# Performance work log

Hardware: AMD Instinct MI355X
Metric: run time of the kernel (lower is better)

The kernel has to match this reference:

```python
import jax, jax.numpy as jnp
import numpy as np

N_PART = 2048
N_BINS = 16
N_FREQS = 8
N_BLOCKS = 4
N_HEADS = 8
DIM = 256
HID = 512
LOWER = 0.0
UPPER = 1.0
FIXED_IDXS = np.array([0, 1])
CHANGED_IDXS = np.array([2])
N_FIXED = 2
N_CHANGED = 1
EMB_IN = 2 * N_FREQS * N_FIXED + 3   # 35
AFF_OUT = N_CHANGED * (3 * N_BINS + 1)  # 49
MIN_BIN = 1e-4
MIN_SLOPE = 1e-4


def _mlp(x, W0, b0, W1, b1, W2, b2):
    # equinox MLP: depth=2 hidden layers, relu activation, identity final
    x = jax.nn.relu(x @ W0.T + b0)
    x = jax.nn.relu(x @ W1.T + b1)
    return x @ W2.T + b2


def _attention(x, Wq, Wk, bk, Wv, Wo, bo):
    # eqx.nn.MultiheadAttention: query bias off, key bias on, value bias off, output bias on
    S, D = x.shape
    dh = D // N_HEADS
    q = (x @ Wq.T).reshape(S, N_HEADS, dh)
    k = (x @ Wk.T + bk).reshape(S, N_HEADS, dh)
    v = (x @ Wv.T).reshape(S, N_HEADS, dh)
    logits = jnp.einsum('shd,thd->hst', q, k) / float(np.sqrt(dh))
    attn = jax.nn.softmax(logits, axis=-1)
    o = jnp.einsum('hst,thd->shd', attn, v).reshape(S, D)
    return o @ Wo.T + bo


def _circular(x, lower, upper, n_freqs):
    # periodic sin/cos embedding of coordinates on [lower, upper)
    freqs = 2.0 * jnp.pi * jnp.arange(1, n_freqs + 1, dtype=x.dtype) / (upper - lower)
    ang = (x - lower)[..., None] * freqs  # (rows, n_fixed, n_freqs)
    feats = jnp.concatenate([jnp.cos(ang), jnp.sin(ang)], axis=-1)
    return feats.reshape(x.shape[0], -1)  # (rows, 2*n_freqs*n_fixed)


def _rqs_forward(x, params):
    # distrax-style rational quadratic spline, boundary_slopes='circular'
    nb = N_BINS
    uw = params[..., :nb]
    uh = params[..., nb:2 * nb]
    ud = params[..., 2 * nb:]
    ud = jnp.concatenate([ud[..., :-1], ud[..., :1]], axis=-1)  # circular: last slope = first
    total = UPPER - LOWER
    widths = jax.nn.softmax(uw, axis=-1) * (total - nb * MIN_BIN) + MIN_BIN
    heights = jax.nn.softmax(uh, axis=-1) * (total - nb * MIN_BIN) + MIN_BIN
    offset = float(np.log(np.expm1(1.0 - MIN_SLOPE)))  # softplus(0+offset)+min = 1
    slopes = jax.nn.softplus(ud + offset) + MIN_SLOPE
    zero = jnp.zeros(widths.shape[:-1] + (1,), widths.dtype)
    xpos = LOWER + jnp.concatenate([zero, jnp.cumsum(widths, -1)], -1)   # (..., nb+1)
    ypos = LOWER + jnp.concatenate([zero, jnp.cumsum(heights, -1)], -1)
    inside = (x >= LOWER) & (x <= UPPER)
    xc = jnp.clip(x, LOWER, UPPER)
    k = jnp.clip(jnp.sum(xc[..., None] >= xpos, axis=-1) - 1, 0, nb - 1)
    g = lambda a: jnp.take_along_axis(a, k[..., None], axis=-1)[..., 0]
    xk, xk1 = g(xpos[..., :-1]), g(xpos[..., 1:])
    yk, yk1 = g(ypos[..., :-1]), g(ypos[..., 1:])
    dk, dk1 = g(slopes[..., :-1]), g(slopes[..., 1:])
    w = xk1 - xk
    h = yk1 - yk
    s = h / w
    z = (xc - xk) / w
    z1 = 1.0 - z
    den = s + (dk1 + dk - 2.0 * s) * z * z1
    y = yk + h * (s * z * z + dk * z * z1) / den
    logdet = 2.0 * jnp.log(s) + jnp.log(dk1 * z * z + 2.0 * s * z * z1 + dk * z1 * z1) - 2.0 * jnp.log(den)
    y = jnp.where(inside, y, x)
    logdet = jnp.where(inside, logdet, 0.0)
    return y, logdet


def _forward(pos, scale, press, temp,
             e_w0, e_b0, e_w1, e_b1, e_w2, e_b2,
             Wq, Wk, bk, Wv, Wo, bo,
             mw0, mb0, mw1, mb1, mw2, mb2,
             a_w0, a_b0, a_w1, a_b1, a_w2, a_b2):
    fixed = pos[1:, FIXED_IDXS]      # (N-1, 2)
    changed = pos[1:, CHANGED_IDXS]  # (N-1, 1)
    feats = _circular(fixed[:, FIXED_IDXS], LOWER, UPPER, N_FREQS)  # (N-1, 32)
    rows = feats.shape[0]
    ones = jnp.ones((rows, 1), feats.dtype)
    cond = jnp.concatenate([feats, ones * scale, ones * temp, ones * press], axis=-1)  # (N-1, 35)
    h = _mlp(cond, e_w0, e_b0, e_w1, e_b1, e_w2, e_b2)  # (N-1, DIM)
    for i in range(N_BLOCKS):
        h = h + _attention(h, Wq[i], Wk[i], bk[i], Wv[i], Wo[i], bo[i])
        h = h + _mlp(h, mw0[i], mb0[i], mw1[i], mb1[i], mw2[i], mb2[i])
    params = _mlp(h, a_w0, a_b0, a_w1, a_b1, a_w2, a_b2)
    params = params.reshape(N_PART - 1, N_CHANGED, 3 * N_BINS + 1)
    y, logdet = _rqs_forward(changed, params)
    pos = pos.at[1:, CHANGED_IDXS].set(y.reshape(N_PART - 1, N_CHANGED))
    return pos, logdet.sum()


def setup_inputs():
    kit = iter(jax.random.split(jax.random.key(0), 40))
    nk = lambda: next(kit)
    def W(out_d, in_d, pre=()):
        return jax.random.normal(nk(), pre + (out_d, in_d), jnp.float32) / np.sqrt(in_d)
    def b(out_d, pre=()):
        return 0.01 * jax.random.normal(nk(), pre + (out_d,), jnp.float32)
    B = (N_BLOCKS,)
    return dict(
        pos=jax.random.uniform(nk(), (N_PART, 3), jnp.float32),
        scale=jax.random.uniform(nk(), (), jnp.float32),
        press=jax.random.uniform(nk(), (), jnp.float32),
        temp=jax.random.uniform(nk(), (), jnp.float32),
        e_w0=W(HID, EMB_IN), e_b0=b(HID),
        e_w1=W(HID, HID), e_b1=b(HID),
        e_w2=W(DIM, HID), e_b2=b(DIM),
        Wq=W(DIM, DIM, B), Wk=W(DIM, DIM, B), bk=b(DIM, B),
        Wv=W(DIM, DIM, B), Wo=W(DIM, DIM, B), bo=b(DIM, B),
        mw0=W(HID, DIM, B), mb0=b(HID, B),
        mw1=W(HID, HID, B), mb1=b(HID, B),
        mw2=W(DIM, HID, B), mb2=b(DIM, B),
        a_w0=W(HID, DIM), a_b0=b(HID),
        a_w1=W(HID, HID), a_b1=b(HID),
        a_w2=W(AFF_OUT, HID), a_b2=b(AFF_OUT),
    )


def reference(pos, scale, press, temp,
              e_w0, e_b0, e_w1, e_b1, e_w2, e_b2,
              Wq, Wk, bk, Wv, Wo, bo,
              mw0, mb0, mw1, mb1, mw2, mb2,
              a_w0, a_b0, a_w1, a_b1, a_w2, a_b2):
    return _forward(pos, scale, press, temp,
                    e_w0, e_b0, e_w1, e_b1, e_w2, e_b2,
                    Wq, Wk, bk, Wv, Wo, bo,
                    mw0, mb0, mw1, mb1, mw2, mb2,
                    a_w0, a_b0, a_w1, a_b1, a_w2, a_b2)
```

## Files before the change

### kernel.cpp

```cpp
#include <hip/hip_runtime.h>
#include <math.h>

#define S_ROWS 2047
#define DIM 256
#define HID 512
#define NHEADS 8
#define DH 32
#define NBINS 16
#define AFF_OUT 49

typedef short bf16x8 __attribute__((ext_vector_type(8)));
typedef float f32x4 __attribute__((ext_vector_type(4)));
typedef float f32x16 __attribute__((ext_vector_type(16)));
typedef unsigned short u16x8 __attribute__((ext_vector_type(8)));
typedef unsigned short u16x4 __attribute__((ext_vector_type(4)));

__device__ inline unsigned short f2b(float f) {
    unsigned int u = __float_as_uint(f);
    u += 0x7FFFu + ((u >> 16) & 1u);
    return (unsigned short)(u >> 16);
}

#define W_MAIN 3957248
#define EW0P_N 32768
#define P0 (W_MAIN / 4)
#define P1 (P0 + EW0P_N / 4)
#define P2 (P1 + 2048 * 64 / 4)
#define P3 (P2 + 1537)
__global__ __launch_bounds__(256) void setup_kernel(
    const float* __restrict__ pos, const float* __restrict__ scale,
    const float* __restrict__ press, const float* __restrict__ temp,
    const float* __restrict__ e_w0, const float* __restrict__ p0,
    const float* __restrict__ p1, const float* __restrict__ p2,
    const float* __restrict__ p3, const float* __restrict__ p4,
    const float* __restrict__ p5, const float* __restrict__ p6,
    const float* __restrict__ p7, const float* __restrict__ p8,
    const float* __restrict__ p9, const float* __restrict__ p10,
    const float* __restrict__ p11, unsigned short* __restrict__ dst,
    unsigned short* __restrict__ cond, float* __restrict__ out)
{
    const int offs[13] = {0, 262144, 393216, 655360, 917504, 1179648, 1441792,
                          1966080, 3014656, 3538944, 3670016, 3932160, 3957248};
    const float* srcs[12] = {p0,p1,p2,p3,p4,p5,p6,p7,p8,p9,p10,p11};
    for (int i4 = blockIdx.x * blockDim.x + threadIdx.x; i4 < P3;
         i4 += gridDim.x * blockDim.x) {
        if (i4 < P0) {
            int e = i4 * 4;
            int s = 0;
            #pragma unroll
            for (int j = 1; j < 12; j++) s += (e >= offs[j]);
            const float4 v = *(const float4*)(srcs[s] + (e - offs[s]));
            u16x4 o;
            o[0] = f2b(v.x); o[1] = f2b(v.y); o[2] = f2b(v.z); o[3] = f2b(v.w);
            *(u16x4*)(dst + EW0P_N + e) = o;
        } else if (i4 < P1) {
            int e = (i4 - P0) * 4;
            u16x4 o;
            #pragma unroll
            for (int r = 0; r < 4; r++) {
                int ee = e + r;
                int row = ee >> 6, col = ee & 63;
                o[r] = (col < 35) ? f2b(e_w0[row * 35 + col]) : (unsigned short)0;
            }
            *(u16x4*)(dst + e) = o;
        } else if (i4 < P2) {
            int e = (i4 - P1) * 4;
            int row = e >> 6;
            u16x4 o;
            #pragma unroll
            for (int r = 0; r < 4; r++) {
                int c = (e + r) & 63;
                float v = 0.f;
                if (row < S_ROWS) {
                    if (c < 32) {
                        int coord = c >> 4;
                        int w = c & 15;
                        float x = pos[(row + 1) * 3 + coord];
                        float f = 6.283185307179586f * (float)((w & 7) + 1);
                        float ang = x * f;
                        v = (w < 8) ? cosf(ang) : sinf(ang);
                    } else if (c == 32) v = scale[0];
                    else if (c == 33) v = temp[0];
                    else if (c == 34) v = press[0];
                }
                o[r] = f2b(v);
            }
            *(u16x4*)(cond + e) = o;
        } else {
            int e = (i4 - P2) * 4;
            #pragma unroll
            for (int r = 0; r < 4; r++) {
                int ee = e + r;
                if (ee < 6144) out[ee] = pos[ee];
                else if (ee == 6144) out[ee] = 0.f;
            }
        }
    }
}

#define LDK 72
__global__ __launch_bounds__(256, 4) void gemm_bf16(
    const unsigned short* __restrict__ Ab, const unsigned short* __restrict__ W,
    const float* __restrict__ bias, const float* resF,
    float* Cf, unsigned short* Cb, int M, int K, int relu)
{
    __shared__ unsigned short As[32][LDK];
    __shared__ unsigned short Bs[32][LDK];
    int tid = threadIdx.x;
    int wave = tid >> 6, lane = tid & 63;
    int quad = lane >> 4, l16 = lane & 15;
    int rowf = (wave & 1) << 4, colf = (wave >> 1) << 4;
    int row0 = blockIdx.y << 5, col0 = blockIdx.x << 5;
    int srow = tid >> 3, scol = (tid & 7) << 3;

    f32x4 acc = {0.f, 0.f, 0.f, 0.f};

    const u16x8* ap = (const u16x8*)(Ab + (size_t)(row0 + srow) * K + scol);
    const u16x8* wp = (const u16x8*)(W + (size_t)(col0 + srow) * K + scol);
    u16x8 a0 = ap[0];
    u16x8 b0 = wp[0];

    for (int k0 = 0; k0 < K; k0 += 64) {
        *(u16x8*)&As[srow][scol] = a0;
        *(u16x8*)&Bs[srow][scol] = b0;
        __syncthreads();
        if (k0 + 64 < K) {
            ap += 8; wp += 8;
            a0 = ap[0]; b0 = wp[0];
        }
        #pragma unroll
        for (int kt = 0; kt < 64; kt += 32) {
            bf16x8 af = *(bf16x8*)&As[rowf + l16][kt + (quad << 3)];
            bf16x8 bf = *(bf16x8*)&Bs[colf + l16][kt + (quad << 3)];
            acc = __builtin_amdgcn_mfma_f32_16x16x32_bf16(af, bf, acc, 0, 0, 0);
        }
        __syncthreads();
    }
    int col = col0 + colf + l16;
    if (col < M) {
        float bv = bias ? bias[col] : 0.f;
        #pragma unroll
        for (int r = 0; r < 4; r++) {
            int row = row0 + rowf + (quad << 2) + r;
            if (row >= S_ROWS) continue;
            float v = acc[r] + bv;
            if (resF) v += resF[(size_t)row * M + col];
            if (relu) v = fmaxf(v, 0.f);
            if (Cf) Cf[(size_t)row * M + col] = v;
            if (Cb) Cb[(size_t)row * M + col] = f2b(v);
        }
    }
}

__global__ __launch_bounds__(256, 4) void gemm_qkv(
    const unsigned short* __restrict__ Ab, const unsigned short* __restrict__ Wq,
    const unsigned short* __restrict__ Wk, const unsigned short* __restrict__ Wv,
    const float* __restrict__ bk,
    unsigned short* __restrict__ qbh, unsigned short* __restrict__ kbh,
    unsigned short* __restrict__ vbT)
{
    __shared__ unsigned short As[32][LDK];
    __shared__ unsigned short Bs[32][LDK];
    const int N = S_ROWS, K = 256;
    int tid = threadIdx.x;
    int wave = tid >> 6, lane = tid & 63;
    int quad = lane >> 4, l16 = lane & 15;
    int rowf = (wave & 1) << 4, colf = (wave >> 1) << 4;
    int row0 = blockIdx.y << 5, col0 = blockIdx.x << 5;
    int mode = col0 >> 8;
    int wcol0 = col0 & 255;
    const unsigned short* W = (mode == 0) ? Wq : (mode == 1) ? Wk : Wv;
    int srow = tid >> 3, scol = (tid & 7) << 3;

    f32x4 acc = {0.f, 0.f, 0.f, 0.f};

    const u16x8* ap = (const u16x8*)(Ab + (size_t)(row0 + srow) * K + scol);
    const u16x8* wp = (const u16x8*)(W + (size_t)(wcol0 + srow) * K + scol);
    u16x8 a0 = ap[0];
    u16x8 b0 = wp[0];

    for (int k0 = 0; k0 < K; k0 += 64) {
        *(u16x8*)&As[srow][scol] = a0;
        *(u16x8*)&Bs[srow][scol] = b0;
        __syncthreads();
        if (k0 + 64 < K) {
            ap += 8; wp += 8;
            a0 = ap[0]; b0 = wp[0];
        }
        #pragma unroll
        for (int kt = 0; kt < 64; kt += 32) {
            bf16x8 af = *(bf16x8*)&As[rowf + l16][kt + (quad << 3)];
            bf16x8 bf = *(bf16x8*)&Bs[colf + l16][kt + (quad << 3)];
            acc = __builtin_amdgcn_mfma_f32_16x16x32_bf16(af, bf, acc, 0, 0, 0);
        }
        __syncthreads();
    }
    int colr = wcol0 + colf + l16;
    int hh = colr >> 5, d = colr & 31;
    int rbase = row0 + rowf + (quad << 2);
    if (mode == 2) {
        unsigned short* dst = vbT + ((size_t)hh * 32 + d) * 2048 + rbase;
        if (rbase + 3 < N) {
            u16x4 o;
            #pragma unroll
            for (int r = 0; r < 4; r++) o[r] = f2b(acc[r]);
            *(u16x4*)dst = o;
        } else {
            #pragma unroll
            for (int r = 0; r < 4; r++)
                if (rbase + r < N) dst[r] = f2b(acc[r]);
        }
    } else {
        float bias = (mode == 1) ? bk[colr] : 0.f;
        unsigned short* dst = ((mode == 0) ? qbh : kbh) + (size_t)hh * 2048 * 32 + d;
        #pragma unroll
        for (int r = 0; r < 4; r++) {
            int row = rbase + r;
            if (row < N) {
                float v = acc[r] + bias;
                if (mode == 0) v *= 0.25506362f;
                dst[(size_t)row * 32] = f2b(v);
            }
        }
    }
}

__global__ __launch_bounds__(256, 2) void attn_mfma(
    const unsigned short* __restrict__ qbh,
    const unsigned short* __restrict__ kbh,
    const unsigned short* __restrict__ vbT,
    unsigned short* __restrict__ obb)
{
    int tid = threadIdx.x;
    int w = tid >> 6;
    int lane = tid & 63;
    int l31 = lane & 31, hf = lane >> 5;
    int q0 = blockIdx.x << 5;
    int h = blockIdx.y;
    int kstart = w * 512;
    int kend = min(kstart + 512, S_ROWS);

    const unsigned short* qp = qbh + ((size_t)h * 2048 + (q0 + l31)) * 32 + hf * 8;
    bf16x8 qf0 = *(const bf16x8*)(qp);
    bf16x8 qf1 = *(const bf16x8*)(qp + 16);

    const unsigned short* kb_h = kbh + (size_t)h * 2048 * 32;
    const unsigned short* vb_h = vbT + ((size_t)h * 32 + l31) * 2048;

    f32x16 acc = {};
    float m = -1e30f, l = 0.f;

    for (int key0 = kstart; key0 < kend; key0 += 32) {
        const unsigned short* kp = kb_h + (size_t)(key0 + l31) * 32 + hf * 8;
        bf16x8 kf0 = *(const bf16x8*)(kp);
        bf16x8 kf1 = *(const bf16x8*)(kp + 16);
        bf16x8 vf0 = *(const bf16x8*)(vb_h + key0 + hf * 8);
        bf16x8 vf1 = *(const bf16x8*)(vb_h + key0 + 16 + hf * 8);

        f32x16 sc = {};
        sc = __builtin_amdgcn_mfma_f32_32x32x16_bf16(kf0, qf0, sc, 0, 0, 0);
        sc = __builtin_amdgcn_mfma_f32_32x32x16_bf16(kf1, qf1, sc, 0, 0, 0);

        if (key0 + 32 > kend) {
            #pragma unroll
            for (int r = 0; r < 16; r++) {
                int kr = key0 + (r & 3) + 8 * (r >> 2) + 4 * hf;
                if (kr >= kend) sc[r] = -1e30f;
            }
        }
        float tmax = sc[0];
        #pragma unroll
        for (int r = 1; r < 16; r++) tmax = fmaxf(tmax, sc[r]);
        tmax = fmaxf(tmax, __shfl_xor(tmax, 32, 64));
        float mnew = fmaxf(m, tmax);
        float corr = __builtin_amdgcn_exp2f(m - mnew);
        m = mnew;
        float p[16];
        float ls = 0.f;
        #pragma unroll
        for (int r = 0; r < 16; r++) {
            p[r] = __builtin_amdgcn_exp2f(sc[r] - mnew);
            ls += p[r];
        }
        ls += __shfl_xor(ls, 32, 64);
        l = l * corr + ls;
        if (__ballot(corr != 1.0f)) {
            #pragma unroll
            for (int r = 0; r < 16; r++) acc[r] *= corr;
        }
        unsigned int pk[8];
        #pragma unroll
        for (int i = 0; i < 8; i++)
            pk[i] = __builtin_amdgcn_perm(__float_as_uint(p[2*i+1]),
                                          __float_as_uint(p[2*i]), 0x07060302u);
        unsigned int x[8];
        #pragma unroll
        for (int i = 0; i < 8; i++)
            x[i] = (unsigned int)__shfl_xor((int)pk[i], 32, 64);
        union { unsigned int u[4]; bf16x8 v; } B1, B2;
        B1.u[0] = hf ? x[2]  : pk[0];
        B1.u[1] = hf ? x[3]  : pk[1];
        B1.u[2] = hf ? pk[2] : x[0];
        B1.u[3] = hf ? pk[3] : x[1];
        B2.u[0] = hf ? x[6]  : pk[4];
        B2.u[1] = hf ? x[7]  : pk[5];
        B2.u[2] = hf ? pk[6] : x[4];
        B2.u[3] = hf ? pk[7] : x[5];
        acc = __builtin_amdgcn_mfma_f32_32x32x16_bf16(vf0, B1.v, acc, 0, 0, 0);
        acc = __builtin_amdgcn_mfma_f32_32x32x16_bf16(vf1, B2.v, acc, 0, 0, 0);
    }

    __shared__ float sm_m[4][32];
    __shared__ float sm_l[4][32];
    __shared__ float sm_acc[4][32][36];
    if (!hf) { sm_m[w][l31] = m; sm_l[w][l31] = l; }
    #pragma unroll
    for (int g = 0; g < 4; g++) {
        float4 o4;
        o4.x = acc[4*g]; o4.y = acc[4*g+1]; o4.z = acc[4*g+2]; o4.w = acc[4*g+3];
        *(float4*)&sm_acc[w][l31][8*g + 4*hf] = o4;
    }
    __syncthreads();

    int q = tid & 31;
    int dg = tid >> 5;
    float mmax = fmaxf(fmaxf(sm_m[0][q], sm_m[1][q]),
                       fmaxf(sm_m[2][q], sm_m[3][q]));
    float lsum = 0.f;
    float num0 = 0.f, num1 = 0.f, num2 = 0.f, num3 = 0.f;
    #pragma unroll
    for (int c = 0; c < 4; c++) {
        float wgt = __builtin_amdgcn_exp2f(sm_m[c][q] - mmax);
        lsum += sm_l[c][q] * wgt;
        float4 o4 = *(const float4*)&sm_acc[c][q][dg * 4];
        num0 = fmaf(o4.x, wgt, num0);
        num1 = fmaf(o4.y, wgt, num1);
        num2 = fmaf(o4.z, wgt, num2);
        num3 = fmaf(o4.w, wgt, num3);
    }
    float inv = 1.f / lsum;
    if (q0 + q < S_ROWS) {
        u16x4 st;
        st[0] = f2b(num0 * inv); st[1] = f2b(num1 * inv);
        st[2] = f2b(num2 * inv); st[3] = f2b(num3 * inv);
        *(u16x4*)(obb + (size_t)(q0 + q) * DIM + h * DH + dg * 4) = st;
    }
}

__global__ __launch_bounds__(64) void spline_kernel(const float* __restrict__ pos,
    const float* __restrict__ params, float* __restrict__ out)
{
    int r = blockIdx.x * 64 + threadIdx.x;
    float ld = 0.f;
    if (r < S_ROWS) {
        const float* p = params + (size_t)r * AFF_OUT;
        float x = pos[(r + 1) * 3 + 2];
        float xc = fminf(fmaxf(x, 0.f), 1.f);

        float mw = -1e30f, mh = -1e30f;
        #pragma unroll
        for (int j = 0; j < NBINS; j++) {
            mw = fmaxf(mw, p[j]);
            mh = fmaxf(mh, p[NBINS + j]);
        }
        float sw = 0.f, sh = 0.f;
        #pragma unroll
        for (int j = 0; j < NBINS; j++) {
            sw += __expf(p[j] - mw);
            sh += __expf(p[NBINS + j] - mh);
        }
        const float span = 1.0f - NBINS * 1e-4f;
        float scw = span / sw, sch = span / sh;

        float cumw = 0.f, cumh = 0.f;
        float xk = 0.f, yk = 0.f, wk = 0.f, hk = 0.f;
        int k = 0;
        #pragma unroll
        for (int j = 0; j < NBINS; j++) {
            float wj = __expf(p[j] - mw) * scw + 1e-4f;
            float hj = __expf(p[NBINS + j] - mh) * sch + 1e-4f;
            if (xc >= cumw) { k = j; xk = cumw; yk = cumh; wk = wj; hk = hj; }
            cumw += wj; cumh += hj;
        }
        float offset = logf(expm1f(0.9999f));
        float t0 = p[2 * NBINS + k] + offset;
        float t1 = ((k == NBINS - 1) ? p[2 * NBINS] : p[2 * NBINS + k + 1]) + offset;
        float dk  = ((t0 > 15.f) ? t0 : log1pf(__expf(t0))) + 1e-4f;
        float dk1 = ((t1 > 15.f) ? t1 : log1pf(__expf(t1))) + 1e-4f;

        float sl = hk / wk;
        float z = (xc - xk) / wk;
        float z1 = 1.f - z;
        float den = sl + (dk1 + dk - 2.f * sl) * z * z1;
        float y = yk + hk * (sl * z * z + dk * z * z1) / den;
        float ldv = 2.f * logf(sl)
                  + logf(dk1 * z * z + 2.f * sl * z * z1 + dk * z1 * z1)
                  - 2.f * logf(den);
        bool inside = (x >= 0.f) && (x <= 1.f);
        y = inside ? y : x;
        ld = inside ? ldv : 0.f;
        out[(r + 1) * 3 + 2] = y;
    }
    #pragma unroll
    for (int st = 32; st > 0; st >>= 1) ld += __shfl_xor(ld, st, 64);
    if (threadIdx.x == 0) atomicAdd(&out[6144], ld);
}

extern "C" void kernel_launch(void* const* d_in, const int* in_sizes, int n_in,
                              void* d_out, int out_size, void* d_ws, size_t ws_size,
                              hipStream_t stream)
{
    const float* pos   = (const float*)d_in[0];
    const float* scale = (const float*)d_in[1];
    const float* press = (const float*)d_in[2];
    const float* temp  = (const float*)d_in[3];
    const float* e_w0  = (const float*)d_in[4];
    const float* e_b0  = (const float*)d_in[5];
    const float* e_w1  = (const float*)d_in[6];
    const float* e_b1  = (const float*)d_in[7];
    const float* e_w2  = (const float*)d_in[8];
    const float* e_b2  = (const float*)d_in[9];
    const float* Wq    = (const float*)d_in[10];
    const float* Wk    = (const float*)d_in[11];
    const float* bk    = (const float*)d_in[12];
    const float* Wv    = (const float*)d_in[13];
    const float* Wo    = (const float*)d_in[14];
    const float* bo    = (const float*)d_in[15];
    const float* mw0   = (const float*)d_in[16];
    const float* mb0   = (const float*)d_in[17];
    const float* mw1   = (const float*)d_in[18];
    const float* mb1   = (const float*)d_in[19];
    const float* mw2   = (const float*)d_in[20];
    const float* mb2   = (const float*)d_in[21];
    const float* a_w0  = (const float*)d_in[22];
    const float* a_b0  = (const float*)d_in[23];
    const float* a_w1  = (const float*)d_in[24];
    const float* a_b1  = (const float*)d_in[25];
    const float* a_w2  = (const float*)d_in[26];
    const float* a_b2  = (const float*)d_in[27];
    float* out = (float*)d_out;

    enum { OFF_EW0 = 0,
           OFF_EW1 = 32768 + 0,       OFF_EW2 = 32768 + 262144,
           OFF_WQ  = 32768 + 393216,  OFF_WK  = 32768 + 655360,
           OFF_WV  = 32768 + 917504,  OFF_WO  = 32768 + 1179648,
           OFF_MW0 = 32768 + 1441792, OFF_MW1 = 32768 + 1966080,
           OFF_MW2 = 32768 + 3014656, OFF_AW0 = 32768 + 3538944,
           OFF_AW1 = 32768 + 3670016, OFF_AW2 = 32768 + 3932160 };
    const size_t WB_U16 = (size_t)EW0P_N + W_MAIN;

    float* ws = (float*)d_ws;
    size_t off = 0;
    float* hbuf = ws + off; off += 2048 * 256;
    float* pr   = ws + off; off += 2048 * 64;
    unsigned short* wbp   = (unsigned short*)(ws + off); off += WB_U16 / 2;
    unsigned short* cond  = (unsigned short*)(ws + off); off += 2048 * 64 / 2;
    unsigned short* t1b   = (unsigned short*)(ws + off); off += 2048 * 512 / 2;
    unsigned short* t2b   = (unsigned short*)(ws + off); off += 2048 * 512 / 2;
    unsigned short* hb    = (unsigned short*)(ws + off); off += 2048 * 256 / 2;
    unsigned short* obb   = (unsigned short*)(ws + off); off += 2048 * 256 / 2;
    unsigned short* qbh   = (unsigned short*)(ws + off); off += NHEADS * 2048 * 32 / 2;
    unsigned short* kbh   = (unsigned short*)(ws + off); off += NHEADS * 2048 * 32 / 2;
    unsigned short* vbT   = (unsigned short*)(ws + off); off += NHEADS * 2048 * 32 / 2;
    (void)ws_size;

    hipLaunchKernelGGL(setup_kernel, dim3(1024), dim3(256), 0, stream,
                       pos, scale, press, temp, e_w0,
                       e_w1, e_w2, Wq, Wk, Wv, Wo, mw0, mw1, mw2,
                       a_w0, a_w1, a_w2, wbp, cond, out);

    auto gemm = [&](const unsigned short* A, const unsigned short* W,
                    const float* bias, const float* resF, float* Cf,
                    unsigned short* Cb, int M, int K, int relu) {
        dim3 grid((M + 31) / 32, 64);
        hipLaunchKernelGGL(gemm_bf16, grid, dim3(256), 0, stream,
                           A, W, bias, resF, Cf, Cb, M, K, relu);
    };

    gemm(cond, wbp + OFF_EW0, e_b0, nullptr, nullptr, t1b, 512, 64, 1);
    gemm(t1b,  wbp + OFF_EW1, e_b1, nullptr, nullptr, t2b, 512, 512, 1);
    gemm(t2b,  wbp + OFF_EW2, e_b2, nullptr, hbuf, hb, 256, 512, 0);

    for (int l = 0; l < 4; l++) {
        hipLaunchKernelGGL(gemm_qkv, dim3(24, 64), dim3(256), 0, stream,
                           hb, wbp + OFF_WQ + l * 65536, wbp + OFF_WK + l * 65536,
                           wbp + OFF_WV + l * 65536, bk + l * 256, qbh, kbh, vbT);
        hipLaunchKernelGGL(attn_mfma, dim3(64, NHEADS), dim3(256), 0, stream,
                           qbh, kbh, vbT, obb);
        gemm(obb, wbp + OFF_WO + l * 65536, bo + l * 256, hbuf, hbuf, hb, 256, 256, 0);
        gemm(hb,  wbp + OFF_MW0 + l * 131072, mb0 + l * 512, nullptr, nullptr, t1b, 512, 256, 1);
        gemm(t1b, wbp + OFF_MW1 + l * 262144, mb1 + l * 512, nullptr, nullptr, t2b, 512, 512, 1);
        gemm(t2b, wbp + OFF_MW2 + l * 131072, mb2 + l * 256, hbuf, hbuf, hb, 256, 512, 0);
    }

    gemm(hb,  wbp + OFF_AW0, a_b0, nullptr, nullptr, t1b, 512, 256, 1);
    gemm(t1b, wbp + OFF_AW1, a_b1, nullptr, nullptr, t2b, 512, 512, 1);
    gemm(t2b, wbp + OFF_AW2, a_b2, nullptr, pr, nullptr, AFF_OUT, 512, 0);

    hipLaunchKernelGGL(spline_kernel, dim3(32), dim3(64), 0, stream, pos, pr, out);
}
```

Measured before the change: 343.1 us.

## Use K=128 tiles in GEMMs and split attention keys across 8 waves

```diff
diff --git a/kernel.cpp b/kernel.cpp
--- a/kernel.cpp
+++ b/kernel.cpp
@@ -99,7 +99,7 @@
 }
 
 #define LDK 72
-__global__ __launch_bounds__(256, 4) void gemm_bf16(
+__global__ __launch_bounds__(256, 4) void gemm_bf16_64(
     const unsigned short* __restrict__ Ab, const unsigned short* __restrict__ W,
     const float* __restrict__ bias, const float* resF,
     float* Cf, unsigned short* Cb, int M, int K, int relu)
@@ -152,6 +152,63 @@
     }
 }
 
+#define LDW 136
+__global__ __launch_bounds__(256, 4) void gemm_bf16_128(
+    const unsigned short* __restrict__ Ab, const unsigned short* __restrict__ W,
+    const float* __restrict__ bias, const float* resF,
+    float* Cf, unsigned short* Cb, int M, int K, int relu)
+{
+    __shared__ unsigned short As[32][LDW];
+    __shared__ unsigned short Bs[32][LDW];
+    int tid = threadIdx.x;
+    int wave = tid >> 6, lane = tid & 63;
+    int quad = lane >> 4, l16 = lane & 15;
+    int rowf = (wave & 1) << 4, colf = (wave >> 1) << 4;
+    int row0 = blockIdx.y << 5, col0 = blockIdx.x << 5;
+    int srow = tid >> 3, scol = (tid & 7) << 4;
+
+    f32x4 acc = {0.f, 0.f, 0.f, 0.f};
+
+    const u16x8* ap = (const u16x8*)(Ab + (size_t)(row0 + srow) * K + scol);
+    const u16x8* wp = (const u16x8*)(W + (size_t)(col0 + srow) * K + scol);
+    u16x8 a0 = ap[0], a1 = ap[1];
+    u16x8 b0 = wp[0], b1 = wp[1];
+
+    for (int k0 = 0; k0 < K; k0 += 128) {
+        *(u16x8*)&As[srow][scol]     = a0;
+        *(u16x8*)&As[srow][scol + 8] = a1;
+        *(u16x8*)&Bs[srow][scol]     = b0;
+        *(u16x8*)&Bs[srow][scol + 8] = b1;
+        __syncthreads();
+        if (k0 + 128 < K) {
+            ap += 16; wp += 16;
+            a0 = ap[0]; a1 = ap[1];
+            b0 = wp[0]; b1 = wp[1];
+        }
+        #pragma unroll
+        for (int kt = 0; kt < 128; kt += 32) {
+            bf16x8 af = *(bf16x8*)&As[rowf + l16][kt + (quad << 3)];
+            bf16x8 bf = *(bf16x8*)&Bs[colf + l16][kt + (quad << 3)];
+            acc = __builtin_amdgcn_mfma_f32_16x16x32_bf16(af, bf, acc, 0, 0, 0);
+        }
+        __syncthreads();
+    }
+    int col = col0 + colf + l16;
+    if (col < M) {
+        float bv = bias ? bias[col] : 0.f;
+        #pragma unroll
+        for (int r = 0; r < 4; r++) {
+            int row = row0 + rowf + (quad << 2) + r;
+            if (row >= S_ROWS) continue;
+            float v = acc[r] + bv;
+            if (resF) v += resF[(size_t)row * M + col];
+            if (relu) v = fmaxf(v, 0.f);
+            if (Cf) Cf[(size_t)row * M + col] = v;
+            if (Cb) Cb[(size_t)row * M + col] = f2b(v);
+        }
+    }
+}
+
 __global__ __launch_bounds__(256, 4) void gemm_qkv(
     const unsigned short* __restrict__ Ab, const unsigned short* __restrict__ Wq,
     const unsigned short* __restrict__ Wk, const unsigned short* __restrict__ Wv,
@@ -159,8 +216,8 @@
     unsigned short* __restrict__ qbh, unsigned short* __restrict__ kbh,
     unsigned short* __restrict__ vbT)
 {
-    __shared__ unsigned short As[32][LDK];
-    __shared__ unsigned short Bs[32][LDK];
+    __shared__ unsigned short As[32][LDW];
+    __shared__ unsigned short Bs[32][LDW];
     const int N = S_ROWS, K = 256;
     int tid = threadIdx.x;
     int wave = tid >> 6, lane = tid & 63;
@@ -170,25 +227,28 @@
     int mode = col0 >> 8;
     int wcol0 = col0 & 255;
     const unsigned short* W = (mode == 0) ? Wq : (mode == 1) ? Wk : Wv;
-    int srow = tid >> 3, scol = (tid & 7) << 3;
+    int srow = tid >> 3, scol = (tid & 7) << 4;
 
     f32x4 acc = {0.f, 0.f, 0.f, 0.f};
 
     const u16x8* ap = (const u16x8*)(Ab + (size_t)(row0 + srow) * K + scol);
     const u16x8* wp = (const u16x8*)(W + (size_t)(wcol0 + srow) * K + scol);
-    u16x8 a0 = ap[0];
-    u16x8 b0 = wp[0];
-
-    for (int k0 = 0; k0 < K; k0 += 64) {
-        *(u16x8*)&As[srow][scol] = a0;
-        *(u16x8*)&Bs[srow][scol] = b0;
+    u16x8 a0 = ap[0], a1 = ap[1];
+    u16x8 b0 = wp[0], b1 = wp[1];
+
+    for (int k0 = 0; k0 < K; k0 += 128) {
+        *(u16x8*)&As[srow][scol]     = a0;
+        *(u16x8*)&As[srow][scol + 8] = a1;
+        *(u16x8*)&Bs[srow][scol]     = b0;
+        *(u16x8*)&Bs[srow][scol + 8] = b1;
         __syncthreads();
-        if (k0 + 64 < K) {
-            ap += 8; wp += 8;
-            a0 = ap[0]; b0 = wp[0];
-        }
-        #pragma unroll
-        for (int kt = 0; kt < 64; kt += 32) {
+        if (k0 + 128 < K) {
+            ap += 16; wp += 16;
+            a0 = ap[0]; a1 = ap[1];
+            b0 = wp[0]; b1 = wp[1];
+        }
+        #pragma unroll
+        for (int kt = 0; kt < 128; kt += 32) {
             bf16x8 af = *(bf16x8*)&As[rowf + l16][kt + (quad << 3)];
             bf16x8 bf = *(bf16x8*)&Bs[colf + l16][kt + (quad << 3)];
             acc = __builtin_amdgcn_mfma_f32_16x16x32_bf16(af, bf, acc, 0, 0, 0);
@@ -225,7 +285,7 @@
     }
 }
 
-__global__ __launch_bounds__(256, 2) void attn_mfma(
+__global__ __launch_bounds__(512, 2) void attn_mfma(
     const unsigned short* __restrict__ qbh,
     const unsigned short* __restrict__ kbh,
     const unsigned short* __restrict__ vbT,
@@ -237,8 +297,8 @@
     int l31 = lane & 31, hf = lane >> 5;
     int q0 = blockIdx.x << 5;
     int h = blockIdx.y;
-    int kstart = w * 512;
-    int kend = min(kstart + 512, S_ROWS);
+    int kstart = w * 256;
+    int kend = min(kstart + 256, S_ROWS);
 
     const unsigned short* qp = qbh + ((size_t)h * 2048 + (q0 + l31)) * 32 + hf * 8;
     bf16x8 qf0 = *(const bf16x8*)(qp);
@@ -310,9 +370,9 @@
         acc = __builtin_amdgcn_mfma_f32_32x32x16_bf16(vf1, B2.v, acc, 0, 0, 0);
     }
 
-    __shared__ float sm_m[4][32];
-    __shared__ float sm_l[4][32];
-    __shared__ float sm_acc[4][32][36];
+    __shared__ float sm_m[8][32];
+    __shared__ float sm_l[8][32];
+    __shared__ float sm_acc[8][32][36];
     if (!hf) { sm_m[w][l31] = m; sm_l[w][l31] = l; }
     #pragma unroll
     for (int g = 0; g < 4; g++) {
@@ -322,28 +382,31 @@
     }
     __syncthreads();
 
-    int q = tid & 31;
-    int dg = tid >> 5;
-    float mmax = fmaxf(fmaxf(sm_m[0][q], sm_m[1][q]),
-                       fmaxf(sm_m[2][q], sm_m[3][q]));
-    float lsum = 0.f;
-    float num0 = 0.f, num1 = 0.f, num2 = 0.f, num3 = 0.f;
-    #pragma unroll
-    for (int c = 0; c < 4; c++) {
-        float wgt = __builtin_amdgcn_exp2f(sm_m[c][q] - mmax);
-        lsum += sm_l[c][q] * wgt;
-        float4 o4 = *(const float4*)&sm_acc[c][q][dg * 4];
-        num0 = fmaf(o4.x, wgt, num0);
-        num1 = fmaf(o4.y, wgt, num1);
-        num2 = fmaf(o4.z, wgt, num2);
-        num3 = fmaf(o4.w, wgt, num3);
-    }
-    float inv = 1.f / lsum;
-    if (q0 + q < S_ROWS) {
-        u16x4 st;
-        st[0] = f2b(num0 * inv); st[1] = f2b(num1 * inv);
-        st[2] = f2b(num2 * inv); st[3] = f2b(num3 * inv);
-        *(u16x4*)(obb + (size_t)(q0 + q) * DIM + h * DH + dg * 4) = st;
+    if (tid < 256) {
+        int q = tid & 31;
+        int dg = tid >> 5;
+        float mmax = -1e30f;
+        #pragma unroll
+        for (int c = 0; c < 8; c++) mmax = fmaxf(mmax, sm_m[c][q]);
+        float lsum = 0.f;
+        float num0 = 0.f, num1 = 0.f, num2 = 0.f, num3 = 0.f;
+        #pragma unroll
+        for (int c = 0; c < 8; c++) {
+            float wgt = __builtin_amdgcn_exp2f(sm_m[c][q] - mmax);
+            lsum += sm_l[c][q] * wgt;
+            float4 o4 = *(const float4*)&sm_acc[c][q][dg * 4];
+            num0 = fmaf(o4.x, wgt, num0);
+            num1 = fmaf(o4.y, wgt, num1);
+            num2 = fmaf(o4.z, wgt, num2);
+            num3 = fmaf(o4.w, wgt, num3);
+        }
+        float inv = 1.f / lsum;
+        if (q0 + q < S_ROWS) {
+            u16x4 st;
+            st[0] = f2b(num0 * inv); st[1] = f2b(num1 * inv);
+            st[2] = f2b(num2 * inv); st[3] = f2b(num3 * inv);
+            *(u16x4*)(obb + (size_t)(q0 + q) * DIM + h * DH + dg * 4) = st;
+        }
     }
 }
 
@@ -473,8 +536,12 @@
                     const float* bias, const float* resF, float* Cf,
                     unsigned short* Cb, int M, int K, int relu) {
         dim3 grid((M + 31) / 32, 64);
-        hipLaunchKernelGGL(gemm_bf16, grid, dim3(256), 0, stream,
-                           A, W, bias, resF, Cf, Cb, M, K, relu);
+        if (K % 128 == 0)
+            hipLaunchKernelGGL(gemm_bf16_128, grid, dim3(256), 0, stream,
+                               A, W, bias, resF, Cf, Cb, M, K, relu);
+        else
+            hipLaunchKernelGGL(gemm_bf16_64, grid, dim3(256), 0, stream,
+                               A, W, bias, resF, Cf, Cb, M, K, relu);
     };
 
     gemm(cond, wbp + OFF_EW0, e_b0, nullptr, nullptr, t1b, 512, 64, 1);
@@ -485,7 +552,7 @@
         hipLaunchKernelGGL(gemm_qkv, dim3(24, 64), dim3(256), 0, stream,
                            hb, wbp + OFF_WQ + l * 65536, wbp + OFF_WK + l * 65536,
                            wbp + OFF_WV + l * 65536, bk + l * 256, qbh, kbh, vbT);
-        hipLaunchKernelGGL(attn_mfma, dim3(64, NHEADS), dim3(256), 0, stream,
+        hipLaunchKernelGGL(attn_mfma, dim3(64, NHEADS), dim3(512), 0, stream,
                            qbh, kbh, vbT, obb);
         gemm(obb, wbp + OFF_WO + l * 65536, bo + l * 256, hbuf, hbuf, hb, 256, 256, 0);
         gemm(hb,  wbp + OFF_MW0 + l * 131072, mb0 + l * 512, nullptr, nullptr, t1b, 512, 256, 1);
```

New measurement: 338.9 us. About the same (-1.2%).
